# Kernel tuning notes

Hardware: AMD Instinct MI355X
Metric: run time of the kernel (lower is better)

Reference implementation:

```python
import jax, jax.numpy as jnp
import numpy as np

T_MAX = 4
TOP_K = 4
TEMP = 1.0
THRESH = 0.99
EPS = 1e-6


def _to_c(x):
    return x[..., 0] + 1j * x[..., 1]


def _from_c(z):
    return jnp.stack([z.real, z.imag], axis=-1)


def _forward(psi, bank_keys, bank_vals, u_halt, W_halt, b_halt, head_mix, out_scale):
    B, T, d, _ = psi.shape
    H = bank_keys.shape[0]
    psi_flat = psi.reshape(B * T, d, 2)
    BT = psi_flat.shape[0]
    psi_h = jnp.broadcast_to(psi_flat[:, None], (BT, H, d, 2))
    cum = jnp.zeros((BT, H), psi.dtype)
    halted = jnp.zeros((BT, H), bool)
    cost = jnp.zeros((BT, H), psi.dtype)
    acc = jnp.zeros((BT, H, d, 2), psi.dtype)
    # normalized halt target vectors u (OrthoHalt)
    uc = _to_c(u_halt)  # [H,d] complex
    un = uc / jnp.sqrt(jnp.sum(uc.real**2 + uc.imag**2, -1, keepdims=True) + EPS)
    hidx = jnp.arange(H)
    for it in range(T_MAX):  # fixed small reasoning depth (structural loop)
        is_last = it == T_MAX - 1
        psi_pool = psi_h.mean(axis=1)                       # [BT,d,2]
        feat = psi_pool.reshape(BT, 2 * d)
        # effect-bank probe + top-k gather
        scores = jnp.einsum('bf,hnf->bhn', feat, bank_keys) / TEMP
        w = jax.nn.softmax(scores, axis=-1)                 # [BT,H,N]
        topw, topi = jax.lax.top_k(w, TOP_K)                # [BT,H,K]
        vecs = bank_vals[hidx[None, :, None], topi]         # [BT,H,K,d,2]
        U = _to_c(vecs) * topw[..., None].astype(jnp.complex64)  # weighted basis
        # rank-K Sasaki projection: Pi_F psi = A (A^H A)^{-1} A^H psi, A = U^T
        psic = _to_c(psi_h)                                 # [BT,H,d]
        m = jnp.einsum('bhkd,bhd->bhk', jnp.conj(U), psic)
        G = jnp.einsum('bhkd,bhjd->bhkj', jnp.conj(U), U)
        G = G + EPS * jnp.eye(TOP_K, dtype=G.dtype)
        coeff = jnp.linalg.solve(G, m[..., None])[..., 0]
        proj = jnp.einsum('bhkd,bhk->bhd', U, coeff)
        psi_next = _from_c(proj)
        # renormalize_psi
        sq = (psi_next[..., 0] ** 2 + psi_next[..., 1] ** 2).sum(-1, keepdims=True)
        psi_next = psi_next / jnp.sqrt(jnp.maximum(sq, 1e-6))[..., None]
        # OrthoHalt on pooled next state -> (alpha, beta, gamma) -> 3 logits
        pool_next = _to_c(psi_next.mean(axis=1))            # [BT,d]
        c = jnp.einsum('hd,bd->bh', jnp.conj(un), pool_next)
        ns = jnp.sum(pool_next.real**2 + pool_next.imag**2, -1)[:, None] + EPS
        alpha = (c.real**2 + c.imag**2) / ns
        beta = 1.0 - alpha
        gamma = c.real**2 / ns
        abg = jnp.stack([alpha, beta, gamma], -1)           # [BT,H,3]
        logits = jnp.einsum('bhi,hij->bhj', abg, W_halt) + b_halt
        probs = jax.nn.softmax(logits, -1)
        p_halt = probs[..., 0] + probs[..., 1]              # yes + no mass
        # ACT ponder update
        would = cum + p_halt
        halts_now = jnp.logical_or(would >= THRESH, is_last)
        active = jnp.logical_not(halted)
        weight = jnp.where(active, jnp.where(halts_now, 1.0 - cum, p_halt), 0.0)
        cost = cost + jnp.where(active, p_halt, 0.0)
        cum = jnp.where(jnp.logical_and(active, jnp.logical_not(halts_now)), would, cum)
        halted = jnp.logical_or(halted, jnp.logical_and(active, halts_now))
        acc = acc + weight[..., None, None] * psi_next
        psi_h = psi_next
    head_w = jax.nn.softmax(head_mix)[None, :, None, None]
    merged = (acc * head_w).sum(axis=1)                     # [BT,d,2]
    residual = merged - psi_flat
    psi_out = (psi_flat + out_scale * residual).reshape(B, T, d, 2)
    return psi_out, cost.mean()


def setup_inputs() -> dict:
    key = jax.random.key(0)
    ks = jax.random.split(key, 6)
    B, T, d, H, N = 2, 2048, 512, 4, 2048
    psi = jax.random.normal(ks[0], (B, T, d, 2), jnp.float32)
    psi = psi / jnp.sqrt(jnp.maximum((psi**2).sum((-1, -2), keepdims=True), 1e-6))
    bank_keys = 0.05 * jax.random.normal(ks[1], (H, N, 2 * d), jnp.float32)
    bank_vals = jax.random.normal(ks[2], (H, N, d, 2), jnp.float32)
    u_halt = jax.random.normal(ks[3], (H, d, 2), jnp.float32)
    W_halt = jax.random.normal(ks[4], (H, 3, 3), jnp.float32)
    b_halt = jnp.zeros((H, 3), jnp.float32)
    head_mix = jnp.zeros((H,), jnp.float32)
    out_scale = jnp.asarray(0.1, jnp.float32)
    return dict(psi=psi, bank_keys=bank_keys, bank_vals=bank_vals, u_halt=u_halt,
                W_halt=W_halt, b_halt=b_halt, head_mix=head_mix, out_scale=out_scale)


def reference(psi, bank_keys, bank_vals, u_halt, W_halt, b_halt, head_mix, out_scale):
    return _forward(psi, bank_keys, bank_vals, u_halt, W_halt, b_halt, head_mix, out_scale)
```

## Files before the change

kernel.cpp:

```cpp
#include <hip/hip_runtime.h>
#include <math.h>

#define HH 4
#define DD 512
#define FF 1024
#define NN 2048
#define KK 4
#define TMAXI 4
#define THRESHV 0.99f
#define EPSV 1e-6f

typedef unsigned short ushort_t;
typedef __attribute__((ext_vector_type(8))) __bf16 bf16x8;
typedef __attribute__((ext_vector_type(4))) float f32x4;
typedef __attribute__((ext_vector_type(4))) unsigned short us4;

__device__ __forceinline__ unsigned short f2bf(float x) {
    unsigned int u = __float_as_uint(x);
    unsigned int r = (u + 0x7FFF + ((u >> 16) & 1)) >> 16;
    return (unsigned short)r;
}

__device__ __forceinline__ float fast_rcp(float x) { return __builtin_amdgcn_rcpf(x); }
__device__ __forceinline__ float fast_rsq(float x) { return __builtin_amdgcn_rsqf(x); }

typedef __attribute__((address_space(3))) unsigned int lds_u32;
typedef __attribute__((address_space(1))) const unsigned int glb_u32;
__device__ __forceinline__ void gl_lds16(const void* g, void* s) {
    __builtin_amdgcn_global_load_lds((glb_u32*)g, (lds_u32*)s, 16, 0, 0);
}

__global__ void k_unorm(const float* __restrict__ u_halt, float* __restrict__ norm_inv) {
    __shared__ float red[256];
    int tid = threadIdx.x;
    for (int h = 0; h < HH; ++h) {
        float s = 0.f;
        for (int i = tid; i < FF; i += 256) { float v = u_halt[h * FF + i]; s += v * v; }
        red[tid] = s; __syncthreads();
        for (int off = 128; off > 0; off >>= 1) {
            if (tid < off) red[tid] += red[tid + off];
            __syncthreads();
        }
        if (tid == 0) norm_inv[h] = 1.0f / sqrtf(red[0] + EPSV);
        __syncthreads();
    }
}

__global__ void k_cvt_bf(const float* __restrict__ in, ushort_t* __restrict__ out, int total) {
    int i = blockIdx.x * 256 + threadIdx.x;
    if (i >= total) return;
    out[i] = f2bf(in[i]);
}

#define BM 128
#define BN 128
#define BKE 32
__global__ __launch_bounds__(256) void k_gemm_mfma(const ushort_t* __restrict__ A,
                                                   const ushort_t* __restrict__ B,
                                                   float* __restrict__ C) {
    __shared__ __align__(16) ushort_t As[BM * BKE];
    __shared__ __align__(16) ushort_t Bs[BN * BKE];
    int tid = threadIdx.x;
    int lane = tid & 63, w = tid >> 6;
    int row0 = blockIdx.y * BM, col0 = blockIdx.x * BN;

    const ushort_t* gA = A + (size_t)(row0 + w * 16 + (lane >> 2)) * FF + (lane & 3) * 8;
    const ushort_t* gB = B + (size_t)(col0 + w * 16 + (lane >> 2)) * FF + (lane & 3) * 8;
    ushort_t* sA = As + (w * 16) * BKE;
    ushort_t* sB = Bs + (w * 16) * BKE;

    int fr = lane & 15;
    int fk = (lane >> 4) * 8;
    int wr0 = (w >> 1) * 64, wc0 = (w & 1) * 64;

    f32x4 acc[4][4] = {};

    for (int kb = 0; kb < FF; kb += BKE) {
        gl_lds16(gA + kb, sA);
        gl_lds16(gA + kb + (size_t)64 * FF, sA + 64 * BKE);
        gl_lds16(gB + kb, sB);
        gl_lds16(gB + kb + (size_t)64 * FF, sB + 64 * BKE);
        __syncthreads();
        bf16x8 af[4], bfv[4];
        #pragma unroll
        for (int i = 0; i < 4; i++) af[i] = *(const bf16x8*)&As[(wr0 + 16 * i + fr) * BKE + fk];
        #pragma unroll
        for (int j = 0; j < 4; j++) bfv[j] = *(const bf16x8*)&Bs[(wc0 + 16 * j + fr) * BKE + fk];
        #pragma unroll
        for (int i = 0; i < 4; i++)
            #pragma unroll
            for (int j = 0; j < 4; j++)
                acc[i][j] = __builtin_amdgcn_mfma_f32_16x16x32_bf16(af[i], bfv[j], acc[i][j], 0, 0, 0);
        __syncthreads();
    }

    int crow = (lane >> 4) * 4;
    int ccol = lane & 15;
    #pragma unroll
    for (int i = 0; i < 4; i++)
        #pragma unroll
        for (int r = 0; r < 4; r++) {
            float* Cr = C + (size_t)(row0 + wr0 + 16 * i + crow + r) * (HH * NN) + col0 + wc0 + ccol;
            #pragma unroll
            for (int j = 0; j < 4; j++) Cr[16 * j] = acc[i][j][r];
        }
}

__global__ __launch_bounds__(256) void k_softtop(const float* __restrict__ Sc,
                                                 float* __restrict__ topw, int* __restrict__ topi,
                                                 int row0) {
    int tid = threadIdx.x;
    int w = tid >> 6, lane = tid & 63;
    int g = blockIdx.x * 4 + w;
    int r = g >> 2;
    int h = g & 3;
    const float* S = Sc + (size_t)r * (HH * NN) + h * NN + lane * 4;
    float4 v[8];
    #pragma unroll
    for (int j = 0; j < 8; j++) v[j] = *(const float4*)(S + 256 * j);

    float bm = v[0].x;
    #pragma unroll
    for (int j = 0; j < 8; j++)
        bm = fmaxf(bm, fmaxf(fmaxf(v[j].x, v[j].y), fmaxf(v[j].z, v[j].w)));
    #pragma unroll
    for (int m = 1; m < 64; m <<= 1) bm = fmaxf(bm, __shfl_xor(bm, m, 64));

    float se = 0.f;
    #pragma unroll
    for (int j = 0; j < 8; j++)
        se += __expf(v[j].x - bm) + __expf(v[j].y - bm) + __expf(v[j].z - bm) + __expf(v[j].w - bm);
    #pragma unroll
    for (int m = 1; m < 64; m <<= 1) se += __shfl_xor(se, m, 64);
    float Zinv = fast_rcp(se);

    int gbh = (row0 + r) * HH + h;
    int base = lane * 4;
    #pragma unroll
    for (int k = 0; k < KK; k++) {
        float bv = -INFINITY; int bi = NN;
        #pragma unroll
        for (int j = 0; j < 8; j++) {
            int n0 = 256 * j + base;
            if (v[j].x > bv) { bv = v[j].x; bi = n0; }
            if (v[j].y > bv) { bv = v[j].y; bi = n0 + 1; }
            if (v[j].z > bv) { bv = v[j].z; bi = n0 + 2; }
            if (v[j].w > bv) { bv = v[j].w; bi = n0 + 3; }
        }
        #pragma unroll
        for (int m = 1; m < 64; m <<= 1) {
            float ov = __shfl_xor(bv, m, 64);
            int   oi = __shfl_xor(bi, m, 64);
            if (ov > bv || (ov == bv && oi < bi)) { bv = ov; bi = oi; }
        }
        if (lane == 0) {
            topw[gbh * KK + k] = __expf(bv - bm) * Zinv;
            topi[gbh * KK + k] = bi;
        }
        if (k < KK - 1) {
            #pragma unroll
            for (int j = 0; j < 8; j++) {
                int n0 = 256 * j + base;
                if (n0     == bi) v[j].x = -INFINITY;
                if (n0 + 1 == bi) v[j].y = -INFINITY;
                if (n0 + 2 == bi) v[j].z = -INFINITY;
                if (n0 + 3 == bi) v[j].w = -INFINITY;
            }
        }
    }
}

__global__ __launch_bounds__(256) void k_fused(const float* __restrict__ psi,
                                               float* __restrict__ psi_h,
                                               const float* __restrict__ bank_vals,
                                               const float* __restrict__ topw,
                                               const int* __restrict__ topi,
                                               const float* __restrict__ u_halt,
                                               const float* __restrict__ norm_inv,
                                               const float* __restrict__ W_halt,
                                               const float* __restrict__ b_halt,
                                               const float* __restrict__ head_mix,
                                               float* __restrict__ merged,
                                               ushort_t* __restrict__ feat,
                                               float* __restrict__ cum,
                                               float* __restrict__ cost,
                                               int* __restrict__ halted,
                                               int first, int is_last) {
    __shared__ float Pn[HH][FF];
    __shared__ float xw[4][9];
    int b = blockIdx.x;
    int tid = threadIdx.x;
    int w = tid >> 6, lane = tid & 63;
    int bh = b * HH + w;

    float wk[KK]; int ix[KK];
    #pragma unroll
    for (int k = 0; k < KK; k++) { wk[k] = topw[bh * KK + k]; ix[k] = topi[bh * KK + k]; }

    const float* Pr = first ? (psi + (size_t)b * FF) : (psi_h + (size_t)bh * FF);
    float4 p4[4], v4[KK][4];
    #pragma unroll
    for (int c = 0; c < 4; c++) p4[c] = *(const float4*)(Pr + lane * 16 + 4 * c);
    #pragma unroll
    for (int k = 0; k < KK; k++) {
        const float* Vp = bank_vals + ((size_t)(w * NN) + ix[k]) * FF + lane * 16;
        #pragma unroll
        for (int c = 0; c < 4; c++) v4[k][c] = *(const float4*)(Vp + 4 * c);
    }

    float part[24];
    #pragma unroll
    for (int t = 0; t < 24; t++) part[t] = 0.f;
    #pragma unroll
    for (int c = 0; c < 4; c++) {
        #pragma unroll
        for (int e = 0; e < 2; e++) {
            float prr = e ? p4[c].z : p4[c].x;
            float pii = e ? p4[c].w : p4[c].y;
            float vr[KK], vi[KK];
            #pragma unroll
            for (int k = 0; k < KK; k++) {
                vr[k] = e ? v4[k][c].z : v4[k][c].x;
                vi[k] = e ? v4[k][c].w : v4[k][c].y;
            }
            #pragma unroll
            for (int k = 0; k < KK; k++) {
                part[2 * k]     += vr[k] * prr + vi[k] * pii;
                part[2 * k + 1] += vr[k] * pii - vi[k] * prr;
                part[8 + k]     += vr[k] * vr[k] + vi[k] * vi[k];
            }
            int t = 12;
            #pragma unroll
            for (int k = 0; k < KK; k++)
                #pragma unroll
                for (int j = k + 1; j < KK; j++) {
                    part[t]     += vr[k] * vr[j] + vi[k] * vi[j];
                    part[t + 1] += vr[k] * vi[j] - vi[k] * vr[j];
                    t += 2;
                }
        }
    }
    #pragma unroll
    for (int m = 1; m < 64; m <<= 1)
        #pragma unroll
        for (int t = 0; t < 24; t++) part[t] += __shfl_xor(part[t], m, 64);

    float mr[KK], mi[KK], Gr[KK][KK], Gi[KK][KK];
    #pragma unroll
    for (int k = 0; k < KK; k++) {
        mr[k] = part[2 * k] * wk[k];
        mi[k] = part[2 * k + 1] * wk[k];
        Gr[k][k] = part[8 + k] * wk[k] * wk[k] + EPSV;
        Gi[k][k] = 0.f;
    }
    {
        int t = 12;
        #pragma unroll
        for (int k = 0; k < KK; k++)
            #pragma unroll
            for (int j = k + 1; j < KK; j++) {
                float s = wk[k] * wk[j];
                Gr[k][j] = part[t] * s;  Gi[k][j] = part[t + 1] * s;
                Gr[j][k] = Gr[k][j];     Gi[j][k] = -Gi[k][j];
                t += 2;
            }
    }

    float Lr[KK][KK], Li[KK][KK], linv[KK];
    #pragma unroll
    for (int j = 0; j < KK; j++) {
        float s = Gr[j][j];
        #pragma unroll
        for (int p = 0; p < KK; p++) if (p < j) s -= Lr[j][p] * Lr[j][p] + Li[j][p] * Li[j][p];
        float ljj = sqrtf(fmaxf(s, 1e-30f));
        Lr[j][j] = ljj; Li[j][j] = 0.f;
        float inv = fast_rcp(ljj);
        linv[j] = inv;
        #pragma unroll
        for (int k = 0; k < KK; k++) {
            if (k > j) {
                float ar = Gr[k][j], ai = Gi[k][j];
                #pragma unroll
                for (int p = 0; p < KK; p++) if (p < j) {
                    ar -= Lr[k][p] * Lr[j][p] + Li[k][p] * Li[j][p];
                    ai -= Li[k][p] * Lr[j][p] - Lr[k][p] * Li[j][p];
                }
                Lr[k][j] = ar * inv; Li[k][j] = ai * inv;
            }
        }
    }
    float yr[KK], yi[KK];
    #pragma unroll
    for (int j = 0; j < KK; j++) {
        float ar = mr[j], ai = mi[j];
        #pragma unroll
        for (int p = 0; p < KK; p++) if (p < j) {
            ar -= Lr[j][p] * yr[p] - Li[j][p] * yi[p];
            ai -= Lr[j][p] * yi[p] + Li[j][p] * yr[p];
        }
        float inv = linv[j];
        yr[j] = ar * inv; yi[j] = ai * inv;
    }
    float xr[KK], xi2[KK];
    #pragma unroll
    for (int j = KK - 1; j >= 0; j--) {
        float ar = yr[j], ai = yi[j];
        #pragma unroll
        for (int p = 0; p < KK; p++) if (p > j) {
            ar -= Lr[p][j] * xr[p] + Li[p][j] * xi2[p];
            ai -= Lr[p][j] * xi2[p] - Li[p][j] * xr[p];
        }
        float inv = linv[j];
        xr[j] = ar * inv; xi2[j] = ai * inv;
    }
    float cxr[KK], cxi[KK];
    #pragma unroll
    for (int k = 0; k < KK; k++) { cxr[k] = xr[k] * wk[k]; cxi[k] = xi2[k] * wk[k]; }

    float4 pj[4];
    float sqp = 0.f;
    #pragma unroll
    for (int c = 0; c < 4; c++) {
        float ar0 = 0.f, ai0 = 0.f, ar1 = 0.f, ai1 = 0.f;
        #pragma unroll
        for (int k = 0; k < KK; k++) {
            ar0 += v4[k][c].x * cxr[k] - v4[k][c].y * cxi[k];
            ai0 += v4[k][c].x * cxi[k] + v4[k][c].y * cxr[k];
            ar1 += v4[k][c].z * cxr[k] - v4[k][c].w * cxi[k];
            ai1 += v4[k][c].z * cxi[k] + v4[k][c].w * cxr[k];
        }
        pj[c].x = ar0; pj[c].y = ai0; pj[c].z = ar1; pj[c].w = ai1;
        sqp += ar0 * ar0 + ai0 * ai0 + ar1 * ar1 + ai1 * ai1;
    }
    #pragma unroll
    for (int m = 1; m < 64; m <<= 1) sqp += __shfl_xor(sqp, m, 64);
    float rn = fast_rsq(fmaxf(sqp, 1e-6f));

    float* Pdst = psi_h + (size_t)bh * FF + lane * 16;
    #pragma unroll
    for (int c = 0; c < 4; c++) {
        float4 o; o.x = pj[c].x * rn; o.y = pj[c].y * rn; o.z = pj[c].z * rn; o.w = pj[c].w * rn;
        *(float4*)(Pdst + 4 * c) = o;
        *(float4*)&Pn[w][lane * 16 + 4 * c] = o;
    }
    __syncthreads();

    int t4 = tid * 4;
    float4 a0 = *(const float4*)&Pn[0][t4];
    float4 a1 = *(const float4*)&Pn[1][t4];
    float4 a2 = *(const float4*)&Pn[2][t4];
    float4 a3 = *(const float4*)&Pn[3][t4];
    float4 pool;
    pool.x = 0.25f * (a0.x + a1.x + a2.x + a3.x);
    pool.y = 0.25f * (a0.y + a1.y + a2.y + a3.y);
    pool.z = 0.25f * (a0.z + a1.z + a2.z + a3.z);
    pool.w = 0.25f * (a0.w + a1.w + a2.w + a3.w);

    float pt[9];
    #pragma unroll
    for (int h = 0; h < HH; h++) {
        float4 u = *(const float4*)&u_halt[h * FF + t4];
        pt[2 * h]     = u.x * pool.x + u.y * pool.y + u.z * pool.z + u.w * pool.w;
        pt[2 * h + 1] = u.x * pool.y - u.y * pool.x + u.z * pool.w - u.w * pool.z;
    }
    pt[8] = pool.x * pool.x + pool.y * pool.y + pool.z * pool.z + pool.w * pool.w;
    #pragma unroll
    for (int m = 1; m < 64; m <<= 1)
        #pragma unroll
        for (int t = 0; t < 9; t++) pt[t] += __shfl_xor(pt[t], m, 64);
    if (lane == 0) {
        #pragma unroll
        for (int t = 0; t < 9; t++) xw[w][t] = pt[t];
    }
    __syncthreads();
    float red[9];
    #pragma unroll
    for (int t = 0; t < 9; t++) red[t] = xw[0][t] + xw[1][t] + xw[2][t] + xw[3][t];
    float ns = red[8] + EPSV;
    float nsinv = fast_rcp(ns);

    float hm0 = head_mix[0], hm1 = head_mix[1], hm2 = head_mix[2], hm3 = head_mix[3];
    float hmx = fmaxf(fmaxf(hm0, hm1), fmaxf(hm2, hm3));
    float he[4] = {__expf(hm0 - hmx), __expf(hm1 - hmx), __expf(hm2 - hmx), __expf(hm3 - hmx)};
    float hsum_inv = fast_rcp(he[0] + he[1] + he[2] + he[3]);

    float wgt[4], addc[4], newcum[4]; int newhl[4];
    int idxb = b * HH;
    #pragma unroll
    for (int h = 0; h < HH; h++) {
        float cr = red[2 * h] * norm_inv[h], ci = red[2 * h + 1] * norm_inv[h];
        float alpha = (cr * cr + ci * ci) * nsinv;
        float beta = 1.0f - alpha;
        float gamma = cr * cr * nsinv;
        float lg[3];
        #pragma unroll
        for (int j = 0; j < 3; j++)
            lg[j] = alpha * W_halt[(h * 3 + 0) * 3 + j] + beta * W_halt[(h * 3 + 1) * 3 + j] +
                    gamma * W_halt[(h * 3 + 2) * 3 + j] + b_halt[h * 3 + j];
        float mx = fmaxf(lg[0], fmaxf(lg[1], lg[2]));
        float e0 = __expf(lg[0] - mx), e1 = __expf(lg[1] - mx), e2 = __expf(lg[2] - mx);
        float p_halt = (e0 + e1) * fast_rcp(e0 + e1 + e2);
        float cm = cum[idxb + h];
        int hl = halted[idxb + h];
        float would = cm + p_halt;
        int halts_now = (would >= THRESHV) || is_last;
        int active = hl ? 0 : 1;
        wgt[h]  = active ? (halts_now ? (1.0f - cm) : p_halt) : 0.0f;
        addc[h] = active ? p_halt : 0.0f;
        newcum[h] = (active && !halts_now) ? would : cm;
        newhl[h]  = hl || (active && halts_now);
    }
    __syncthreads();
    if (tid < HH) {
        cost[idxb + tid] += addc[tid];
        cum[idxb + tid] = newcum[tid];
        halted[idxb + tid] = newhl[tid];
    }
    float hwv[4];
    #pragma unroll
    for (int h = 0; h < HH; h++) hwv[h] = (he[h] * hsum_inv) * wgt[h];

    size_t mo = (size_t)b * FF + t4;
    float4 m4 = *(const float4*)&merged[mo];
    m4.x += hwv[0] * a0.x + hwv[1] * a1.x + hwv[2] * a2.x + hwv[3] * a3.x;
    m4.y += hwv[0] * a0.y + hwv[1] * a1.y + hwv[2] * a2.y + hwv[3] * a3.y;
    m4.z += hwv[0] * a0.z + hwv[1] * a1.z + hwv[2] * a2.z + hwv[3] * a3.z;
    m4.w += hwv[0] * a0.w + hwv[1] * a1.w + hwv[2] * a2.w + hwv[3] * a3.w;
    *(float4*)&merged[mo] = m4;

    us4 fb;
    fb.x = f2bf(pool.x); fb.y = f2bf(pool.y); fb.z = f2bf(pool.z); fb.w = f2bf(pool.w);
    *(us4*)&feat[mo] = fb;
}

__global__ void k_out(const float* __restrict__ psi, const float* __restrict__ merged,
                      const float* __restrict__ out_scale, float* __restrict__ out, int total) {
    int i = blockIdx.x * 256 + threadIdx.x;
    if (i >= total) return;
    float p = psi[i];
    out[i] = p + out_scale[0] * (merged[i] - p);
}

__global__ void k_costmean(const float* __restrict__ cost, float* __restrict__ out, int n) {
    __shared__ float red[256];
    int tid = threadIdx.x;
    float s = 0.f;
    for (int i = tid; i < n; i += 256) s += cost[i];
    red[tid] = s; __syncthreads();
    for (int off = 128; off > 0; off >>= 1) {
        if (tid < off) red[tid] += red[tid + off];
        __syncthreads();
    }
    if (tid == 0) out[0] = red[0] / (float)n;
}

extern "C" void kernel_launch(void* const* d_in, const int* in_sizes, int n_in,
                              void* d_out, int out_size, void* d_ws, size_t ws_size,
                              hipStream_t stream) {
    const float* psi       = (const float*)d_in[0];
    const float* bank_keys = (const float*)d_in[1];
    const float* bank_vals = (const float*)d_in[2];
    const float* u_halt    = (const float*)d_in[3];
    const float* W_halt    = (const float*)d_in[4];
    const float* b_halt    = (const float*)d_in[5];
    const float* head_mix  = (const float*)d_in[6];
    const float* out_scale = (const float*)d_in[7];
    float* out = (float*)d_out;

    const int BT = in_sizes[0] / FF;

    float* ws = (float*)d_ws;
    size_t off = 0;
    float* psi_h  = ws + off; off += (size_t)BT * HH * FF;
    float* merged = ws + off; off += (size_t)BT * FF;
    float* cum    = ws + off; off += (size_t)BT * HH;
    float* costv  = ws + off; off += (size_t)BT * HH;
    int*   halted = (int*)(ws + off); off += (size_t)BT * HH;
    float* topw   = ws + off; off += (size_t)BT * HH * KK;
    int*   topi   = (int*)(ws + off); off += (size_t)BT * HH * KK;
    float* norminv = ws + off; off += 16;
    ushort_t* feat_bf = (ushort_t*)(ws + off); off += (size_t)BT * FF / 2;
    ushort_t* keys_bf = (ushort_t*)(ws + off); off += (size_t)HH * NN * FF / 2;
    float* scores = ws + off;
    size_t fixed = off;

    size_t ws_floats = ws_size / 4;
    int RC = BT;
    while (RC > 128 && fixed + (size_t)RC * HH * NN > ws_floats) RC >>= 1;
    int nchunks = BT / RC;

    hipMemsetAsync(merged, 0, ((size_t)BT * FF + 3 * (size_t)BT * HH) * sizeof(float), stream);
    k_unorm<<<1, 256, 0, stream>>>(u_halt, norminv);
    int tot_keys = HH * NN * FF;
    k_cvt_bf<<<(tot_keys + 255) / 256, 256, 0, stream>>>(bank_keys, keys_bf, tot_keys);
    int tot_bf = BT * FF;
    k_cvt_bf<<<(tot_bf + 255) / 256, 256, 0, stream>>>(psi, feat_bf, tot_bf);

    for (int it = 0; it < TMAXI; ++it) {
        for (int c = 0; c < nchunks; ++c) {
            k_gemm_mfma<<<dim3((HH * NN) / BN, RC / BM), 256, 0, stream>>>(
                feat_bf + (size_t)c * RC * FF, keys_bf, scores);
            k_softtop<<<dim3((RC * HH) / 4), 256, 0, stream>>>(scores, topw, topi, c * RC);
        }
        k_fused<<<BT, 256, 0, stream>>>(psi, psi_h, bank_vals, topw, topi, u_halt, norminv,
                                        W_halt, b_halt, head_mix, merged, feat_bf,
                                        cum, costv, halted,
                                        (it == 0) ? 1 : 0, (it == TMAXI - 1) ? 1 : 0);
    }
    k_out<<<(tot_bf + 255) / 256, 256, 0, stream>>>(psi, merged, out_scale, out, tot_bf);
    k_costmean<<<1, 256, 0, stream>>>(costv, out + tot_bf, BT * HH);
}
```

Before: 1.113 ms.

## Double GEMM K-tile depth and revert fast reciprocal intrinsics to precise math

The bf16 MFMA score GEMM now stages a 64-wide K slice per iteration instead of 32. That halves the number of barrier-separated loop trips, and each trip issues twice as many MFMAs. The global-to-LDS load mapping is changed to match the new tile shape. Separately, the halting and Cholesky code drops the fast rcp/rsq intrinsics and __expf in favour of exact division, sqrt and expf, which trades a little speed in small per-row kernels for accuracy.

Result: slower. 1.178 ms (+5.8%).

```diff
diff --git a/kernel.cpp b/kernel.cpp
--- a/kernel.cpp
+++ b/kernel.cpp
@@ -20,9 +20,6 @@
     unsigned int r = (u + 0x7FFF + ((u >> 16) & 1)) >> 16;
     return (unsigned short)r;
 }
-
-__device__ __forceinline__ float fast_rcp(float x) { return __builtin_amdgcn_rcpf(x); }
-__device__ __forceinline__ float fast_rsq(float x) { return __builtin_amdgcn_rsqf(x); }
 
 typedef __attribute__((address_space(3))) unsigned int lds_u32;
 typedef __attribute__((address_space(1))) const unsigned int glb_u32;
@@ -54,7 +51,7 @@
 
 #define BM 128
 #define BN 128
-#define BKE 32
+#define BKE 64
 __global__ __launch_bounds__(256) void k_gemm_mfma(const ushort_t* __restrict__ A,
                                                    const ushort_t* __restrict__ B,
                                                    float* __restrict__ C) {
@@ -64,10 +61,10 @@
     int lane = tid & 63, w = tid >> 6;
     int row0 = blockIdx.y * BM, col0 = blockIdx.x * BN;
 
-    const ushort_t* gA = A + (size_t)(row0 + w * 16 + (lane >> 2)) * FF + (lane & 3) * 8;
-    const ushort_t* gB = B + (size_t)(col0 + w * 16 + (lane >> 2)) * FF + (lane & 3) * 8;
-    ushort_t* sA = As + (w * 16) * BKE;
-    ushort_t* sB = Bs + (w * 16) * BKE;
+    const ushort_t* gA = A + (size_t)(row0 + w * 32 + (lane >> 3)) * FF + (lane & 7) * 8;
+    const ushort_t* gB = B + (size_t)(col0 + w * 32 + (lane >> 3)) * FF + (lane & 7) * 8;
+    ushort_t* sA = As + (w * 32) * BKE;
+    ushort_t* sB = Bs + (w * 32) * BKE;
 
     int fr = lane & 15;
     int fk = (lane >> 4) * 8;
@@ -76,21 +73,27 @@
     f32x4 acc[4][4] = {};
 
     for (int kb = 0; kb < FF; kb += BKE) {
-        gl_lds16(gA + kb, sA);
-        gl_lds16(gA + kb + (size_t)64 * FF, sA + 64 * BKE);
-        gl_lds16(gB + kb, sB);
-        gl_lds16(gB + kb + (size_t)64 * FF, sB + 64 * BKE);
+        #pragma unroll
+        for (int i = 0; i < 4; i++) {
+            gl_lds16(gA + kb + (size_t)(8 * i) * FF, sA + (8 * i) * BKE);
+            gl_lds16(gB + kb + (size_t)(8 * i) * FF, sB + (8 * i) * BKE);
+        }
         __syncthreads();
-        bf16x8 af[4], bfv[4];
-        #pragma unroll
-        for (int i = 0; i < 4; i++) af[i] = *(const bf16x8*)&As[(wr0 + 16 * i + fr) * BKE + fk];
-        #pragma unroll
-        for (int j = 0; j < 4; j++) bfv[j] = *(const bf16x8*)&Bs[(wc0 + 16 * j + fr) * BKE + fk];
-        #pragma unroll
-        for (int i = 0; i < 4; i++)
-            #pragma unroll
-            for (int j = 0; j < 4; j++)
-                acc[i][j] = __builtin_amdgcn_mfma_f32_16x16x32_bf16(af[i], bfv[j], acc[i][j], 0, 0, 0);
+        bf16x8 af[2][4], bfv[2][4];
+        #pragma unroll
+        for (int hf = 0; hf < 2; hf++)
+            #pragma unroll
+            for (int i = 0; i < 4; i++) {
+                af[hf][i]  = *(const bf16x8*)&As[(wr0 + 16 * i + fr) * BKE + hf * 32 + fk];
+                bfv[hf][i] = *(const bf16x8*)&Bs[(wc0 + 16 * i + fr) * BKE + hf * 32 + fk];
+            }
+        #pragma unroll
+        for (int hf = 0; hf < 2; hf++)
+            #pragma unroll
+            for (int i = 0; i < 4; i++)
+                #pragma unroll
+                for (int j = 0; j < 4; j++)
+                    acc[i][j] = __builtin_amdgcn_mfma_f32_16x16x32_bf16(af[hf][i], bfv[hf][j], acc[i][j], 0, 0, 0);
         __syncthreads();
     }
 
@@ -132,7 +135,7 @@
         se += __expf(v[j].x - bm) + __expf(v[j].y - bm) + __expf(v[j].z - bm) + __expf(v[j].w - bm);
     #pragma unroll
     for (int m = 1; m < 64; m <<= 1) se += __shfl_xor(se, m, 64);
-    float Zinv = fast_rcp(se);
+    float Zinv = __builtin_amdgcn_rcpf(se);
 
     int gbh = (row0 + r) * HH + h;
     int base = lane * 4;
@@ -266,7 +269,7 @@
             }
     }
 
-    float Lr[KK][KK], Li[KK][KK], linv[KK];
+    float Lr[KK][KK], Li[KK][KK];
     #pragma unroll
     for (int j = 0; j < KK; j++) {
         float s = Gr[j][j];
@@ -274,8 +277,7 @@
         for (int p = 0; p < KK; p++) if (p < j) s -= Lr[j][p] * Lr[j][p] + Li[j][p] * Li[j][p];
         float ljj = sqrtf(fmaxf(s, 1e-30f));
         Lr[j][j] = ljj; Li[j][j] = 0.f;
-        float inv = fast_rcp(ljj);
-        linv[j] = inv;
+        float inv = 1.0f / ljj;
         #pragma unroll
         for (int k = 0; k < KK; k++) {
             if (k > j) {
@@ -298,7 +300,7 @@
             ar -= Lr[j][p] * yr[p] - Li[j][p] * yi[p];
             ai -= Lr[j][p] * yi[p] + Li[j][p] * yr[p];
         }
-        float inv = linv[j];
+        float inv = 1.0f / Lr[j][j];
         yr[j] = ar * inv; yi[j] = ai * inv;
     }
     float xr[KK], xi2[KK];
@@ -310,7 +312,7 @@
             ar -= Lr[p][j] * xr[p] + Li[p][j] * xi2[p];
             ai -= Lr[p][j] * xi2[p] - Li[p][j] * xr[p];
         }
-        float inv = linv[j];
+        float inv = 1.0f / Lr[j][j];
         xr[j] = ar * inv; xi2[j] = ai * inv;
     }
     float cxr[KK], cxi[KK];
@@ -334,7 +336,7 @@
     }
     #pragma unroll
     for (int m = 1; m < 64; m <<= 1) sqp += __shfl_xor(sqp, m, 64);
-    float rn = fast_rsq(fmaxf(sqp, 1e-6f));
+    float rn = 1.0f / sqrtf(fmaxf(sqp, 1e-6f));
 
     float* Pdst = psi_h + (size_t)bh * FF + lane * 16;
     #pragma unroll
@@ -377,29 +379,28 @@
     #pragma unroll
     for (int t = 0; t < 9; t++) red[t] = xw[0][t] + xw[1][t] + xw[2][t] + xw[3][t];
     float ns = red[8] + EPSV;
-    float nsinv = fast_rcp(ns);
 
     float hm0 = head_mix[0], hm1 = head_mix[1], hm2 = head_mix[2], hm3 = head_mix[3];
     float hmx = fmaxf(fmaxf(hm0, hm1), fmaxf(hm2, hm3));
-    float he[4] = {__expf(hm0 - hmx), __expf(hm1 - hmx), __expf(hm2 - hmx), __expf(hm3 - hmx)};
-    float hsum_inv = fast_rcp(he[0] + he[1] + he[2] + he[3]);
+    float he[4] = {expf(hm0 - hmx), expf(hm1 - hmx), expf(hm2 - hmx), expf(hm3 - hmx)};
+    float hsum = he[0] + he[1] + he[2] + he[3];
 
     float wgt[4], addc[4], newcum[4]; int newhl[4];
     int idxb = b * HH;
     #pragma unroll
     for (int h = 0; h < HH; h++) {
         float cr = red[2 * h] * norm_inv[h], ci = red[2 * h + 1] * norm_inv[h];
-        float alpha = (cr * cr + ci * ci) * nsinv;
+        float alpha = (cr * cr + ci * ci) / ns;
         float beta = 1.0f - alpha;
-        float gamma = cr * cr * nsinv;
+        float gamma = cr * cr / ns;
         float lg[3];
         #pragma unroll
         for (int j = 0; j < 3; j++)
             lg[j] = alpha * W_halt[(h * 3 + 0) * 3 + j] + beta * W_halt[(h * 3 + 1) * 3 + j] +
                     gamma * W_halt[(h * 3 + 2) * 3 + j] + b_halt[h * 3 + j];
         float mx = fmaxf(lg[0], fmaxf(lg[1], lg[2]));
-        float e0 = __expf(lg[0] - mx), e1 = __expf(lg[1] - mx), e2 = __expf(lg[2] - mx);
-        float p_halt = (e0 + e1) * fast_rcp(e0 + e1 + e2);
+        float e0 = expf(lg[0] - mx), e1 = expf(lg[1] - mx), e2 = expf(lg[2] - mx);
+        float p_halt = (e0 + e1) / (e0 + e1 + e2);
         float cm = cum[idxb + h];
         int hl = halted[idxb + h];
         float would = cm + p_halt;
@@ -418,7 +419,7 @@
     }
     float hwv[4];
     #pragma unroll
-    for (int h = 0; h < HH; h++) hwv[h] = (he[h] * hsum_inv) * wgt[h];
+    for (int h = 0; h < HH; h++) hwv[h] = (he[h] / hsum) * wgt[h];
 
     size_t mo = (size_t)b * FF + t4;
     float4 m4 = *(const float4*)&merged[mo];
```
